# Kernel tuning notes

Measured on AMD Instinct MI355X. Metric: run time of the kernel, lower is better.

The kernel has to match this reference:

```python
import jax, jax.numpy as jnp
import numpy as np

B, T, F0, N = 16, 64, 8, 100
NEX = 15           # nExchanges -> conv sequence length NEX+1 = 16
F1, F2 = 32, 64    # conv channels
K1, K2 = 4, 3      # filter taps
ALPHA = 2          # pooling size (both layers)
D_RD = 128         # readout input: N_last(2) * F2(64)
H_RD, OUT = 64, 5  # readout hidden / output dims


def setup_inputs() -> dict:
    key = jax.random.key(0)
    ks = jax.random.split(key, 10)
    x = jax.random.normal(ks[0], (B, T, F0, N), jnp.float32)
    S = jax.random.normal(ks[1], (B, T, N, N), jnp.float32) / np.float32(np.sqrt(N))
    conv1_w = jax.random.normal(ks[2], (F1, F0, K1), jnp.float32) * 0.1
    conv1_b = jax.random.normal(ks[3], (F1,), jnp.float32) * 0.1
    conv2_w = jax.random.normal(ks[4], (F2, F1, K2), jnp.float32) * 0.1
    conv2_b = jax.random.normal(ks[5], (F2,), jnp.float32) * 0.1
    fc1_w = jax.random.normal(ks[6], (H_RD, D_RD), jnp.float32) * 0.1
    fc1_b = jax.random.normal(ks[7], (H_RD,), jnp.float32) * 0.1
    fc2_w = jax.random.normal(ks[8], (OUT, H_RD), jnp.float32) * 0.1
    fc2_b = jax.random.normal(ks[9], (OUT,), jnp.float32) * 0.1
    return {"x": x, "S": S, "conv1_w": conv1_w, "conv1_b": conv1_b,
            "conv2_w": conv2_w, "conv2_b": conv2_b,
            "fc1_w": fc1_w, "fc1_b": fc1_b, "fc2_w": fc2_w, "fc2_b": fc2_b}


def _conv1d(u, w, b):
    # u: [M, Cin, L], w: [Cout, Cin, K] -> [M, Cout, L-K+1] (cross-correlation, like torch)
    v = jax.lax.conv_general_dilated(u, w, window_strides=(1,), padding='VALID',
                                     dimension_numbers=('NCH', 'OIH', 'NCH'))
    return v + b[None, :, None]


def _maxpool1d(u, a):
    return jax.lax.reduce_window(u, -jnp.inf, jax.lax.max,
                                 (1, 1, a), (1, 1, a), 'VALID')


def reference(x, S, conv1_w, conv1_b, conv2_w, conv2_b, fc1_w, fc1_b, fc2_w, fc2_b):
    # Delayed-time GSO diffusion: x_k[t] = x_{k-1}[t-1] @ S[t], zero-padded at t=0.
    def step(xc, _):
        xc = jnp.concatenate([jnp.zeros_like(xc[:, :1]), xc[:, :-1]], axis=1)  # time shift
        xc = jnp.einsum('btfn,btnm->btfm', xc, S)
        return xc, xc
    _, xs = jax.lax.scan(step, x, None, length=NEX)          # [NEX, B, T, F0, N]
    z = jnp.concatenate([x[None], xs], axis=0)               # [NEX+1, B, T, F0, N]
    # -> [B*T*N, F0, NEX+1] matching torch permute/reshape ordering (b,t,n) rows
    z = jnp.transpose(z, (1, 2, 4, 3, 0)).reshape(B * T * N, F0, NEX + 1)

    y = _maxpool1d(jax.nn.relu(_conv1d(z, conv1_w, conv1_b)), ALPHA)  # [M, F1, 6]
    y = _maxpool1d(jax.nn.relu(_conv1d(y, conv2_w, conv2_b)), ALPHA)  # [M, F2, 2]
    y = y.reshape(B * T * N, D_RD)
    y = jax.nn.relu(y @ fc1_w.T + fc1_b)
    y = y @ fc2_w.T + fc2_b                                  # [M, OUT]
    return y.reshape(B, T, N, OUT).transpose(0, 1, 3, 2)     # [B, T, OUT, N]
```

## Files before the change

kernel.cpp:

```cpp
#include <hip/hip_runtime.h>

#define BB    16
#define TT    64
#define F0    8
#define NN    100
#define NEX   15
#define F1    32
#define F2    64
#define HRD   64
#define OUTD  5
#define BT    (BB*TT)
#define MROWS (BT*NN)
#define NK    14
#define ZELEMS  ((size_t)BT*F0*NK*NN)
#define Y1ELEMS ((size_t)BT*F1*6*NN)
#define Y2ELEMS ((size_t)BT*128*NN)

__global__ __launch_bounds__(512) void head_chain(
    const float* __restrict__ x, const float* __restrict__ S,
    float* __restrict__ zbuf) {
  __shared__ float Sld[2][NN * NN];
  __shared__ float zl[2][4 * NN * F0];

  const int blk = blockIdx.x;
  const int b   = blk >> 4;
  const int g   = blk & 15;
  const int tb  = 1 + 4 * g;
  const int te  = min(tb + 16, TT - 1);
  const int tid = threadIdx.x;
  const int m   = tid & 127;
  const int c2  = (tid >> 7) & 1;
  const int f0b = (tid >> 8) * 4;

  auto act = [&](int T, int dst) {
    const int c = T - tb;
    if (c >= 0 && c < 4 && T <= TT - 1 && (c & 1) == c2 && m < NN) {
#pragma unroll
      for (int j = 0; j < 4; ++j)
        zl[dst][c * (NN * F0) + m * F0 + f0b + j] =
            x[((size_t)(b * TT + T - 1) * F0 + f0b + j) * NN + m];
    }
  };

  {
    const float4* Sg = (const float4*)(S + (size_t)(b * TT + tb) * NN * NN);
    float4 R[5];
#pragma unroll
    for (int i = 0; i < 5; ++i) {
      int idx = tid + i * 512; if (idx > 2499) idx = 2499;
      R[i] = Sg[idx];
    }
#pragma unroll
    for (int i = 0; i < 5; ++i) {
      const int idx = tid + i * 512;
      if (idx < 2500) *(float4*)&Sld[0][idx * 4] = R[i];
    }
  }
  act(tb, 0);
  __syncthreads();

  int p = 0;
  for (int t = tb; t <= te; ++t, p ^= 1) {
    const bool more = (t < te);
    float4 Rn[5];
    if (more) {
      const float4* Sg =
          (const float4*)(S + (size_t)(b * TT + t + 1) * NN * NN);
#pragma unroll
      for (int i = 0; i < 5; ++i) {
        int idx = tid + i * 512; if (idx > 2499) idx = 2499;
        Rn[i] = Sg[idx];
      }
    }

    const int t0a = tb + c2;
    const int t0b = tb + c2 + 2;
    const bool a0 = (t >= t0a) && (t <= t0a + 13);
    const bool a1 = (t >= t0b) && (t <= t0b + 13) && (t0b <= TT - 1);

    float acc0[4] = {0.f, 0.f, 0.f, 0.f};
    float acc1[4] = {0.f, 0.f, 0.f, 0.f};
    if (m < NN) {
      const float* Sc = Sld[p];
      const float* zA = &zl[p][c2 * (NN * F0) + f0b];
      const float* zB = &zl[p][(c2 + 2) * (NN * F0) + f0b];
      if (a0 && a1) {
#pragma unroll 10
        for (int n = 0; n < NN; ++n) {
          const float s = Sc[n * NN + m];
          const float4 z0 = *(const float4*)&zA[n * F0];
          const float4 z1 = *(const float4*)&zB[n * F0];
          acc0[0] += z0.x * s; acc0[1] += z0.y * s;
          acc0[2] += z0.z * s; acc0[3] += z0.w * s;
          acc1[0] += z1.x * s; acc1[1] += z1.y * s;
          acc1[2] += z1.z * s; acc1[3] += z1.w * s;
        }
      } else if (a0) {
#pragma unroll 10
        for (int n = 0; n < NN; ++n) {
          const float s = Sc[n * NN + m];
          const float4 z0 = *(const float4*)&zA[n * F0];
          acc0[0] += z0.x * s; acc0[1] += z0.y * s;
          acc0[2] += z0.z * s; acc0[3] += z0.w * s;
        }
      } else if (a1) {
#pragma unroll 10
        for (int n = 0; n < NN; ++n) {
          const float s = Sc[n * NN + m];
          const float4 z1 = *(const float4*)&zB[n * F0];
          acc1[0] += z1.x * s; acc1[1] += z1.y * s;
          acc1[2] += z1.z * s; acc1[3] += z1.w * s;
        }
      }
    }

    if (m < NN) {
      if (a0) {
        *(float4*)&zl[p ^ 1][c2 * (NN * F0) + m * F0 + f0b] =
            make_float4(acc0[0], acc0[1], acc0[2], acc0[3]);
        const int k = t - t0a;
#pragma unroll
        for (int j = 0; j < 4; ++j)
          zbuf[(((size_t)(b * TT + t) * F0 + f0b + j) * NK + k) * NN + m] =
              acc0[j];
      }
      if (a1) {
        *(float4*)&zl[p ^ 1][(c2 + 2) * (NN * F0) + m * F0 + f0b] =
            make_float4(acc1[0], acc1[1], acc1[2], acc1[3]);
        const int k = t - t0b;
#pragma unroll
        for (int j = 0; j < 4; ++j)
          zbuf[(((size_t)(b * TT + t) * F0 + f0b + j) * NK + k) * NN + m] =
              acc1[j];
      }
    }
    act(t + 1, p ^ 1);
    if (more) {
#pragma unroll
      for (int i = 0; i < 5; ++i) {
        const int idx = tid + i * 512;
        if (idx < 2500) *(float4*)&Sld[p ^ 1][idx * 4] = Rn[i];
      }
    }
    __syncthreads();
  }
}

__global__ __launch_bounds__(256) void conv1_k(
    const float* __restrict__ x, const float* __restrict__ zbuf,
    const float* __restrict__ w1, const float* __restrict__ b1,
    float* __restrict__ y1g) {
  const int row = blockIdx.x * 256 + threadIdx.x;
  const int bt  = row / NN;
  const int n   = row - bt * NN;
  const int t   = bt & (TT - 1);
  const int c0  = blockIdx.y * 8;

  float acc[8][12];
#pragma unroll
  for (int j = 0; j < 8; ++j) {
    const float bias = b1[c0 + j];
#pragma unroll
    for (int l = 0; l < 12; ++l) acc[j][l] = bias;
  }

#pragma unroll 1
  for (int ci = 0; ci < F0; ++ci) {
    float zv[15];
    zv[0] = x[((size_t)bt * F0 + ci) * NN + n];
#pragma unroll
    for (int k = 1; k < 15; ++k)
      zv[k] = (k <= t)
          ? zbuf[(((size_t)bt * F0 + ci) * NK + (k - 1)) * NN + n]
          : 0.f;
#pragma unroll
    for (int j = 0; j < 8; ++j)
#pragma unroll
      for (int kk = 0; kk < 4; ++kk) {
        const float w = w1[((c0 + j) * F0 + ci) * 4 + kk];
#pragma unroll
        for (int l = 0; l < 12; ++l) acc[j][l] += zv[l + kk] * w;
      }
  }

#pragma unroll
  for (int j = 0; j < 8; ++j)
#pragma unroll
    for (int p = 0; p < 6; ++p)
      y1g[((size_t)bt * (F1 * 6) + (c0 + j) * 6 + p) * NN + n] =
          fmaxf(fmaxf(acc[j][2 * p], acc[j][2 * p + 1]), 0.f);
}

__global__ __launch_bounds__(256) void conv2_k(
    const float* __restrict__ y1g,
    const float* __restrict__ w2, const float* __restrict__ b2,
    float* __restrict__ y2g) {
  const int row = blockIdx.x * 256 + threadIdx.x;
  const int bt  = row / NN;
  const int n   = row - bt * NN;
  const int cc  = blockIdx.y * 16;

  float acc[16][4];
#pragma unroll
  for (int j = 0; j < 16; ++j) {
    const float bb = b2[cc + j];
#pragma unroll
    for (int l = 0; l < 4; ++l) acc[j][l] = bb;
  }

#pragma unroll 1
  for (int ci = 0; ci < F1; ++ci) {
    float yv[6];
#pragma unroll
    for (int l = 0; l < 6; ++l)
      yv[l] = y1g[((size_t)bt * (F1 * 6) + ci * 6 + l) * NN + n];
#pragma unroll
    for (int j = 0; j < 16; ++j)
#pragma unroll
      for (int kk = 0; kk < 3; ++kk) {
        const float w = w2[((cc + j) * F1 + ci) * 3 + kk];
#pragma unroll
        for (int l = 0; l < 4; ++l) acc[j][l] += yv[l + kk] * w;
      }
  }

#pragma unroll
  for (int j = 0; j < 16; ++j) {
    y2g[((size_t)bt * 128 + (cc + j) * 2 + 0) * NN + n] =
        fmaxf(fmaxf(acc[j][0], acc[j][1]), 0.f);
    y2g[((size_t)bt * 128 + (cc + j) * 2 + 1) * NN + n] =
        fmaxf(fmaxf(acc[j][2], acc[j][3]), 0.f);
  }
}

__global__ __launch_bounds__(256) void fc_k(
    const float* __restrict__ y2g,
    const float* __restrict__ fw1, const float* __restrict__ fb1,
    const float* __restrict__ fw2, const float* __restrict__ fb2,
    float* __restrict__ out) {
  const int row = blockIdx.x * 256 + threadIdx.x;
  const int bt  = row / NN;
  const int n   = row - bt * NN;
  const float* yi = y2g + (size_t)bt * 128 * NN + n;

  float v[128];
#pragma unroll
  for (int d = 0; d < 128; ++d) v[d] = yi[(size_t)d * NN];

  float o[OUTD];
#pragma unroll
  for (int q = 0; q < OUTD; ++q) o[q] = fb2[q];

#pragma unroll 1
  for (int j = 0; j < HRD; ++j) {
    const float* wr = fw1 + j * 128;
    float s0 = 0.f, s1 = 0.f, s2 = 0.f, s3 = 0.f;
#pragma unroll
    for (int d = 0; d < 128; d += 4) {
      s0 += v[d + 0] * wr[d + 0];
      s1 += v[d + 1] * wr[d + 1];
      s2 += v[d + 2] * wr[d + 2];
      s3 += v[d + 3] * wr[d + 3];
    }
    const float h = fmaxf((s0 + s1) + (s2 + s3) + fb1[j], 0.f);
#pragma unroll
    for (int q = 0; q < OUTD; ++q) o[q] += h * fw2[q * HRD + j];
  }
#pragma unroll
  for (int q = 0; q < OUTD; ++q)
    out[((size_t)bt * OUTD + q) * NN + n] = o[q];
}

extern "C" void kernel_launch(void* const* d_in, const int* in_sizes, int n_in,
                              void* d_out, int out_size, void* d_ws,
                              size_t ws_size, hipStream_t stream) {
  const float* x   = (const float*)d_in[0];
  const float* S   = (const float*)d_in[1];
  const float* w1  = (const float*)d_in[2];
  const float* b1  = (const float*)d_in[3];
  const float* w2  = (const float*)d_in[4];
  const float* b2  = (const float*)d_in[5];
  const float* fw1 = (const float*)d_in[6];
  const float* fb1 = (const float*)d_in[7];
  const float* fw2 = (const float*)d_in[8];
  const float* fb2 = (const float*)d_in[9];

  float* zbuf = (float*)d_ws;
  float* y1g  = zbuf + ZELEMS;
  float* y2g  = y1g + Y1ELEMS;
  float* outp = (float*)d_out;

  head_chain<<<BB * 16, 512, 0, stream>>>(x, S, zbuf);
  conv1_k<<<dim3(MROWS / 256, 4), 256, 0, stream>>>(x, zbuf, w1, b1, y1g);
  conv2_k<<<dim3(MROWS / 256, 4), 256, 0, stream>>>(y1g, w2, b2, y2g);
  fc_k<<<MROWS / 256, 256, 0, stream>>>(y2g, fw1, fb1, fw2, fb2, outp);
}
```

Before: 287.1 us.

## Split head chain into more smaller blocks and widen conv2 channel tile

The diffusion head kernel now runs 512 blocks of 256 threads, each handling two chains instead of four. It single-buffers the S matrix in shared memory and adds an extra barrier around each reload, which cuts shared memory per block so more blocks can be resident. Separately, conv2 now computes 32 output channels per thread instead of 16, halving the grid and the repeated reads of y1. The costs are more redundant S loads across blocks, serialized S stores between barriers, and higher register pressure in conv2 from the 128-element accumulator.

Measured after the change: 313.2 us. 1.09x slower.

```diff
diff --git a/kernel.cpp b/kernel.cpp
--- a/kernel.cpp
+++ b/kernel.cpp
@@ -16,44 +16,37 @@
 #define Y1ELEMS ((size_t)BT*F1*6*NN)
 #define Y2ELEMS ((size_t)BT*128*NN)
 
-__global__ __launch_bounds__(512) void head_chain(
+__global__ __launch_bounds__(256) void head_chain(
     const float* __restrict__ x, const float* __restrict__ S,
     float* __restrict__ zbuf) {
-  __shared__ float Sld[2][NN * NN];
-  __shared__ float zl[2][4 * NN * F0];
+  __shared__ float Sld[NN * NN];
+  __shared__ float zl[2][2 * NN * F0];
 
   const int blk = blockIdx.x;
-  const int b   = blk >> 4;
-  const int g   = blk & 15;
-  const int tb  = 1 + 4 * g;
-  const int te  = min(tb + 16, TT - 1);
+  const int b   = blk >> 5;
+  const int g   = blk & 31;
+  const int tb  = 1 + 2 * g;
+  const int te  = min(tb + 14, TT - 1);
   const int tid = threadIdx.x;
   const int m   = tid & 127;
-  const int c2  = (tid >> 7) & 1;
-  const int f0b = (tid >> 8) * 4;
+  const int f0b = (tid >> 7) * 4;
 
   auto act = [&](int T, int dst) {
     const int c = T - tb;
-    if (c >= 0 && c < 4 && T <= TT - 1 && (c & 1) == c2 && m < NN) {
+    if (c >= 0 && c < 2 && T <= TT - 1 && m < NN) {
 #pragma unroll
       for (int j = 0; j < 4; ++j)
-        zl[dst][c * (NN * F0) + m * F0 + f0b + j] =
+        zl[dst][c * 800 + m * F0 + f0b + j] =
             x[((size_t)(b * TT + T - 1) * F0 + f0b + j) * NN + m];
     }
   };
 
   {
     const float4* Sg = (const float4*)(S + (size_t)(b * TT + tb) * NN * NN);
-    float4 R[5];
-#pragma unroll
-    for (int i = 0; i < 5; ++i) {
-      int idx = tid + i * 512; if (idx > 2499) idx = 2499;
-      R[i] = Sg[idx];
-    }
-#pragma unroll
-    for (int i = 0; i < 5; ++i) {
-      const int idx = tid + i * 512;
-      if (idx < 2500) *(float4*)&Sld[0][idx * 4] = R[i];
+#pragma unroll
+    for (int i = 0; i < 10; ++i) {
+      const int idx = tid + i * 256;
+      if (idx < 2500) *(float4*)&Sld[idx * 4] = Sg[idx];
     }
   }
   act(tb, 0);
@@ -62,32 +55,29 @@
   int p = 0;
   for (int t = tb; t <= te; ++t, p ^= 1) {
     const bool more = (t < te);
-    float4 Rn[5];
+    float4 Rn[10];
     if (more) {
       const float4* Sg =
           (const float4*)(S + (size_t)(b * TT + t + 1) * NN * NN);
 #pragma unroll
-      for (int i = 0; i < 5; ++i) {
-        int idx = tid + i * 512; if (idx > 2499) idx = 2499;
+      for (int i = 0; i < 10; ++i) {
+        int idx = tid + i * 256; if (idx > 2499) idx = 2499;
         Rn[i] = Sg[idx];
       }
     }
 
-    const int t0a = tb + c2;
-    const int t0b = tb + c2 + 2;
-    const bool a0 = (t >= t0a) && (t <= t0a + 13);
-    const bool a1 = (t >= t0b) && (t <= t0b + 13) && (t0b <= TT - 1);
+    const bool a0 = (t - tb <= 13);
+    const bool a1 = (t > tb) && (tb + 1 <= TT - 1);
 
     float acc0[4] = {0.f, 0.f, 0.f, 0.f};
     float acc1[4] = {0.f, 0.f, 0.f, 0.f};
     if (m < NN) {
-      const float* Sc = Sld[p];
-      const float* zA = &zl[p][c2 * (NN * F0) + f0b];
-      const float* zB = &zl[p][(c2 + 2) * (NN * F0) + f0b];
+      const float* zA = &zl[p][f0b];
+      const float* zB = &zl[p][800 + f0b];
       if (a0 && a1) {
 #pragma unroll 10
         for (int n = 0; n < NN; ++n) {
-          const float s = Sc[n * NN + m];
+          const float s = Sld[n * NN + m];
           const float4 z0 = *(const float4*)&zA[n * F0];
           const float4 z1 = *(const float4*)&zB[n * F0];
           acc0[0] += z0.x * s; acc0[1] += z0.y * s;
@@ -98,7 +88,7 @@
       } else if (a0) {
 #pragma unroll 10
         for (int n = 0; n < NN; ++n) {
-          const float s = Sc[n * NN + m];
+          const float s = Sld[n * NN + m];
           const float4 z0 = *(const float4*)&zA[n * F0];
           acc0[0] += z0.x * s; acc0[1] += z0.y * s;
           acc0[2] += z0.z * s; acc0[3] += z0.w * s;
@@ -106,7 +96,7 @@
       } else if (a1) {
 #pragma unroll 10
         for (int n = 0; n < NN; ++n) {
-          const float s = Sc[n * NN + m];
+          const float s = Sld[n * NN + m];
           const float4 z1 = *(const float4*)&zB[n * F0];
           acc1[0] += z1.x * s; acc1[1] += z1.y * s;
           acc1[2] += z1.z * s; acc1[3] += z1.w * s;
@@ -116,18 +106,18 @@
 
     if (m < NN) {
       if (a0) {
-        *(float4*)&zl[p ^ 1][c2 * (NN * F0) + m * F0 + f0b] =
+        *(float4*)&zl[p ^ 1][m * F0 + f0b] =
             make_float4(acc0[0], acc0[1], acc0[2], acc0[3]);
-        const int k = t - t0a;
+        const int k = t - tb;
 #pragma unroll
         for (int j = 0; j < 4; ++j)
           zbuf[(((size_t)(b * TT + t) * F0 + f0b + j) * NK + k) * NN + m] =
               acc0[j];
       }
       if (a1) {
-        *(float4*)&zl[p ^ 1][(c2 + 2) * (NN * F0) + m * F0 + f0b] =
+        *(float4*)&zl[p ^ 1][800 + m * F0 + f0b] =
             make_float4(acc1[0], acc1[1], acc1[2], acc1[3]);
-        const int k = t - t0b;
+        const int k = t - tb - 1;
 #pragma unroll
         for (int j = 0; j < 4; ++j)
           zbuf[(((size_t)(b * TT + t) * F0 + f0b + j) * NK + k) * NN + m] =
@@ -135,14 +125,16 @@
       }
     }
     act(t + 1, p ^ 1);
+
     if (more) {
-#pragma unroll
-      for (int i = 0; i < 5; ++i) {
-        const int idx = tid + i * 512;
-        if (idx < 2500) *(float4*)&Sld[p ^ 1][idx * 4] = Rn[i];
-      }
-    }
-    __syncthreads();
+      __syncthreads();
+#pragma unroll
+      for (int i = 0; i < 10; ++i) {
+        const int idx = tid + i * 256;
+        if (idx < 2500) *(float4*)&Sld[idx * 4] = Rn[i];
+      }
+      __syncthreads();
+    }
   }
 }
 
@@ -198,11 +190,11 @@
   const int row = blockIdx.x * 256 + threadIdx.x;
   const int bt  = row / NN;
   const int n   = row - bt * NN;
-  const int cc  = blockIdx.y * 16;
-
-  float acc[16][4];
-#pragma unroll
-  for (int j = 0; j < 16; ++j) {
+  const int cc  = blockIdx.y * 32;
+
+  float acc[32][4];
+#pragma unroll
+  for (int j = 0; j < 32; ++j) {
     const float bb = b2[cc + j];
 #pragma unroll
     for (int l = 0; l < 4; ++l) acc[j][l] = bb;
@@ -215,7 +207,7 @@
     for (int l = 0; l < 6; ++l)
       yv[l] = y1g[((size_t)bt * (F1 * 6) + ci * 6 + l) * NN + n];
 #pragma unroll
-    for (int j = 0; j < 16; ++j)
+    for (int j = 0; j < 32; ++j)
 #pragma unroll
       for (int kk = 0; kk < 3; ++kk) {
         const float w = w2[((cc + j) * F1 + ci) * 3 + kk];
@@ -225,7 +217,7 @@
   }
 
 #pragma unroll
-  for (int j = 0; j < 16; ++j) {
+  for (int j = 0; j < 32; ++j) {
     y2g[((size_t)bt * 128 + (cc + j) * 2 + 0) * NN + n] =
         fmaxf(fmaxf(acc[j][0], acc[j][1]), 0.f);
     y2g[((size_t)bt * 128 + (cc + j) * 2 + 1) * NN + n] =
@@ -290,8 +282,8 @@
   float* y2g  = y1g + Y1ELEMS;
   float* outp = (float*)d_out;
 
-  head_chain<<<BB * 16, 512, 0, stream>>>(x, S, zbuf);
+  head_chain<<<BB * 32, 256, 0, stream>>>(x, S, zbuf);
   conv1_k<<<dim3(MROWS / 256, 4), 256, 0, stream>>>(x, zbuf, w1, b1, y1g);
-  conv2_k<<<dim3(MROWS / 256, 4), 256, 0, stream>>>(y1g, w2, b2, y2g);
+  conv2_k<<<dim3(MROWS / 256, 2), 256, 0, stream>>>(y1g, w2, b2, y2g);
   fc_k<<<MROWS / 256, 256, 0, stream>>>(y2g, fw1, fb1, fw2, fb2, outp);
 }
```
